# Optimization experiments

Hardware: AMD Instinct MI355X
Metric: run time of the kernel (lower is better)

Reference implementation:

```python
import jax, jax.numpy as jnp
import numpy as np

B, S, D = 4, 2048, 1024
H, DK, DV, DFF = 16, 64, 64, 4096
EPS = 1e-5


def layer_norm(x, g, b):
    mu = jnp.mean(x, axis=-1, keepdims=True)
    var = jnp.mean((x - mu) ** 2, axis=-1, keepdims=True)
    return (x - mu) * jax.lax.rsqrt(var + EPS) * g + b


def setup_inputs() -> dict:
    key = jax.random.key(0)
    ks = jax.random.split(key, 12)
    s = lambda fan_in: 1.0 / np.sqrt(fan_in)
    return {
        "x": jax.random.normal(ks[0], (B, S, D), dtype=jnp.float32),
        # per-head projections stacked: [H, D, DK/DV] (x @ W layout)
        "Wq": jax.random.normal(ks[1], (H, D, DK), dtype=jnp.float32) * s(D),
        "Wk": jax.random.normal(ks[2], (H, D, DK), dtype=jnp.float32) * s(D),
        "Wv": jax.random.normal(ks[3], (H, D, DV), dtype=jnp.float32) * s(D),
        "Wo": jax.random.normal(ks[4], (H * DV, D), dtype=jnp.float32) * s(H * DV),
        "ln1_g": jnp.ones((D,), dtype=jnp.float32),
        "ln1_b": jnp.zeros((D,), dtype=jnp.float32),
        "W1": jax.random.normal(ks[5], (D, DFF), dtype=jnp.float32) * s(D),
        "b1": jnp.zeros((DFF,), dtype=jnp.float32),
        "W2": jax.random.normal(ks[6], (DFF, D), dtype=jnp.float32) * s(DFF),
        "b2": jnp.zeros((D,), dtype=jnp.float32),
        "ln2_g": jnp.ones((D,), dtype=jnp.float32),
        "ln2_b": jnp.zeros((D,), dtype=jnp.float32),
    }


def reference(x, Wq, Wk, Wv, Wo, ln1_g, ln1_b, W1, b1, W2, b2, ln2_g, ln2_b):
    # --- multi-head causal self-attention (all heads vectorized) ---
    q = jnp.einsum("bsd,hdk->bhsk", x, Wq)
    k = jnp.einsum("bsd,hdk->bhsk", x, Wk)
    v = jnp.einsum("bsd,hdv->bhsv", x, Wv)
    # NOTE: original scales by 1/sqrt(x.shape[-1]) == 1/sqrt(d_model)
    scale = 1.0 / np.sqrt(D).astype(np.float32)
    scores = jnp.einsum("bhsk,bhtk->bhst", q, k) * scale  # [B,H,S,S]
    causal = jnp.tril(jnp.ones((S, S), dtype=bool))
    scores = jnp.where(causal, scores, -jnp.inf)
    attn = jax.nn.softmax(scores, axis=-1)
    ctx = jnp.einsum("bhst,bhtv->bhsv", attn, v)  # [B,H,S,DV]
    # concat heads (head-major last dim, matches torch.cat order)
    ctx = ctx.transpose(0, 2, 1, 3).reshape(B, S, H * DV)
    attn_out = ctx @ Wo  # [B,S,D]
    # Sublayer 1 (dropout is identity in eval)
    h1 = layer_norm(x + attn_out, ln1_g, ln1_b)
    # --- FFN ---
    ff = jax.nn.relu(h1 @ W1 + b1) @ W2 + b2
    # Sublayer 2
    return layer_norm(h1 + ff, ln2_g, ln2_b)
```

## Files before the change

### kernel.cpp

```cpp
#include <hip/hip_runtime.h>

#define DEV __device__ __forceinline__

using f16x8 = _Float16 __attribute__((ext_vector_type(8)));
using f16x4 = _Float16 __attribute__((ext_vector_type(4)));
using f32x4 = float __attribute__((ext_vector_type(4)));

DEV f32x4 mfma16(f16x8 a, f16x8 b, f32x4 c) {
    return __builtin_amdgcn_mfma_f32_16x16x32_f16(a, b, c, 0, 0, 0);
}

DEV void gload16(const void* g, void* l) {
    __builtin_amdgcn_global_load_lds(
        (const __attribute__((address_space(1))) void*)g,
        (__attribute__((address_space(3))) void*)l, 16, 0, 0);
}

template <int MODE>
__global__ __launch_bounds__(256, 2) void gemm_bt(
    const _Float16* __restrict__ A, const _Float16* __restrict__ Bt,
    int M, int N, int K,
    const float* __restrict__ ep0, const float* __restrict__ ep1,
    void* __restrict__ o0, void* __restrict__ o1, void* __restrict__ o2)
{
    __shared__ __align__(16) _Float16 As[128 * 64];
    __shared__ __align__(16) _Float16 Bs[128 * 64];
    const int tid  = threadIdx.x;
    const int wave = tid >> 6, lane = tid & 63;
    const int l16  = lane & 15, g = lane >> 4;
    const int m0 = blockIdx.x * 128, n0 = blockIdx.y * 128;
    const int wm = (wave >> 1) * 64, wn = (wave & 1) * 64;

    f32x4 acc[4][4] = {};

    for (int kt = 0; kt < K; kt += 64) {
#pragma unroll
        for (int it = 0; it < 4; ++it) {
            const int off  = it * 4096 + tid * 16;
            const int row  = off >> 7;
            const int colb = (off & 127) ^ ((row & 7) << 4);
            gload16(A + (size_t)(m0 + row) * K + kt + (colb >> 1), (char*)As + off);
        }
#pragma unroll
        for (int it = 0; it < 4; ++it) {
            const int off  = it * 4096 + tid * 16;
            const int row  = off >> 7;
            const int colb = (off & 127) ^ ((row & 7) << 4);
            gload16(Bt + (size_t)(n0 + row) * K + kt + (colb >> 1), (char*)Bs + off);
        }
        __syncthreads();
#pragma unroll
        for (int kk = 0; kk < 2; ++kk) {
            f16x8 af[4], bfv[4];
#pragma unroll
            for (int i = 0; i < 4; ++i) {
                const int ar = wm + i * 16 + l16;
                const int cb = ((kk * 32 + g * 8) << 1) ^ ((ar & 7) << 4);
                af[i] = *(const f16x8*)((const char*)As + (ar << 7) + cb);
            }
#pragma unroll
            for (int j = 0; j < 4; ++j) {
                const int br = wn + j * 16 + l16;
                const int cb = ((kk * 32 + g * 8) << 1) ^ ((br & 7) << 4);
                bfv[j] = *(const f16x8*)((const char*)Bs + (br << 7) + cb);
            }
#pragma unroll
            for (int i = 0; i < 4; ++i)
#pragma unroll
                for (int j = 0; j < 4; ++j)
                    acc[i][j] = mfma16(af[i], bfv[j], acc[i][j]);
        }
        __syncthreads();
    }

#pragma unroll
    for (int i = 0; i < 4; ++i) {
#pragma unroll
        for (int j = 0; j < 4; ++j) {
#pragma unroll
            for (int r = 0; r < 4; ++r) {
                const int m = m0 + wm + i * 16 + g * 4 + r;
                const int n = n0 + wn + j * 16 + l16;
                const float val = acc[i][j][r];
                if constexpr (MODE == 0) {
                    const int b = m >> 11, s = m & 2047;
                    const int which = n >> 10, hh = (n >> 6) & 15, dd = n & 63;
                    const size_t bh = (size_t)(b * 16 + hh);
                    if (which == 0) {
                        ((_Float16*)o0)[(bh * 2048 + s) * 64 + dd] =
                            (_Float16)(val * 0.04508422f);
                    } else if (which == 1) {
                        ((_Float16*)o1)[(bh * 2048 + s) * 64 + dd] = (_Float16)val;
                    } else {
                        ((_Float16*)o2)[(bh * 64 + dd) * 2048 + s] = (_Float16)val;
                    }
                } else if constexpr (MODE == 1) {
                    const size_t idx = (size_t)m * N + n;
                    ((float*)o0)[idx] = val + ep0[idx];
                } else if constexpr (MODE == 2) {
                    float v = val + ep0[n];
                    ((_Float16*)o0)[(size_t)m * N + n] = (_Float16)(v > 0.f ? v : 0.f);
                } else {
                    const size_t idx = (size_t)m * N + n;
                    ((float*)o0)[idx] = val + ep0[n] + ep1[idx];
                }
            }
        }
    }
}

DEV void stage_kv(const _Float16* __restrict__ Kh, const _Float16* __restrict__ Vh,
                  int kb0, char* ksb, char* vsb, int tid)
{
#pragma unroll
    for (int it = 0; it < 2; ++it) {
        const int off  = it * 4096 + tid * 16;
        const int row  = off >> 7;
        const int colb = (off & 127) ^ ((row & 7) << 4);
        gload16(Kh + (size_t)(kb0 + row) * 64 + (colb >> 1), ksb + off);
    }
#pragma unroll
    for (int it = 0; it < 2; ++it) {
        const int off  = it * 4096 + tid * 16;
        const int row  = off >> 7;
        const int colb = (off & 127) ^ ((row & 7) << 4);
        gload16(Vh + (size_t)row * 2048 + kb0 + (colb >> 1), vsb + off);
    }
}

__global__ __launch_bounds__(256, 4) void attn_kernel(
    const _Float16* __restrict__ Q, const _Float16* __restrict__ Kb,
    const _Float16* __restrict__ Vt, _Float16* __restrict__ ctx)
{
    __shared__ __align__(16) char smem[40960];
    const int tid = threadIdx.x;
    const int w = tid >> 6, lane = tid & 63;
    const int l16 = lane & 15, g = lane >> 4;
    const int bh = blockIdx.y;
    const int b = bh >> 4, h = bh & 15;
    const int tA = blockIdx.x;

    const _Float16* Kh = Kb + (size_t)bh * 2048 * 64;
    const _Float16* Vh = Vt + (size_t)bh * 64 * 2048;
    const int swl = (l16 & 7) << 4;
    char* prow = smem + 32768 + w * 2048 + l16 * 128;

    for (int half = 0; half < 2; ++half) {
        const int T = half ? (31 - tA) : tA;
        const int qbase = T * 64 + w * 16;
        const int qg = qbase + l16;
        const int nt = T + 1;

        const _Float16* qrow = Q + ((size_t)bh * 2048 + qg) * 64;
        const f16x8 qf0 = *(const f16x8*)(qrow + g * 8);
        const f16x8 qf1 = *(const f16x8*)(qrow + 32 + g * 8);

        f32x4 cacc[4] = {};
        float m_run = -INFINITY, l_run = 0.f;

        stage_kv(Kh, Vh, 0, smem, smem + 16384, tid);
        if (nt > 1) stage_kv(Kh, Vh, 64, smem + 8192, smem + 24576, tid);

        for (int kt = 0; kt < nt; ++kt) {
            const int bufo = (kt & 1) << 13;
            char* kbuf = smem + bufo;
            char* vbuf = smem + 16384 + bufo;

            if (kt + 1 < nt) asm volatile("s_waitcnt vmcnt(4)" ::: "memory");
            else             asm volatile("s_waitcnt vmcnt(0)" ::: "memory");
            __builtin_amdgcn_s_barrier();
            __builtin_amdgcn_sched_barrier(0);

            f32x4 st[4];
            __builtin_amdgcn_s_setprio(1);
#pragma unroll
            for (int s = 0; s < 4; ++s) {
                const char* kr = kbuf + (16 * s + l16) * 128;
                const f16x8 klo = *(const f16x8*)(kr + ((g * 16) ^ swl));
                const f16x8 khi = *(const f16x8*)(kr + ((64 + g * 16) ^ swl));
                f32x4 a0 = {0.f, 0.f, 0.f, 0.f};
                a0 = mfma16(klo, qf0, a0);
                st[s] = mfma16(khi, qf1, a0);
            }
            __builtin_amdgcn_s_setprio(0);

            if (kt == nt - 1) {
#pragma unroll
                for (int s = 0; s < 4; ++s)
#pragma unroll
                    for (int r = 0; r < 4; ++r) {
                        const int kg = kt * 64 + s * 16 + g * 4 + r;
                        if (kg > qg) st[s][r] = -INFINITY;
                    }
            }

            float tmax = st[0][0];
#pragma unroll
            for (int s = 0; s < 4; ++s)
#pragma unroll
                for (int r = 0; r < 4; ++r) tmax = fmaxf(tmax, st[s][r]);
            tmax = fmaxf(tmax, __shfl_xor(tmax, 16));
            tmax = fmaxf(tmax, __shfl_xor(tmax, 32));

            if (__any(tmax > m_run)) {
                const float m_new = fmaxf(m_run, tmax);
                const float alpha = exp2f(m_run - m_new);
                m_run = m_new;
                l_run *= alpha;
                f32x4 al;
#pragma unroll
                for (int r = 0; r < 4; ++r) al[r] = __shfl(alpha, g * 4 + r);
#pragma unroll
                for (int jt = 0; jt < 4; ++jt)
#pragma unroll
                    for (int r = 0; r < 4; ++r) cacc[jt][r] *= al[r];
            }

            float tsum = 0.f;
#pragma unroll
            for (int s = 0; s < 4; ++s) {
                f16x4 p;
#pragma unroll
                for (int r = 0; r < 4; ++r) {
                    const float e = exp2f(st[s][r] - m_run);
                    tsum += e;
                    p[r] = (_Float16)e;
                }
                *(f16x4*)(prow + ((s * 32 + g * 8) ^ swl)) = p;
            }
            tsum += __shfl_xor(tsum, 16);
            tsum += __shfl_xor(tsum, 32);
            l_run += tsum;

            const f16x8 pf0 = *(const f16x8*)(prow + ((g * 16) ^ swl));
            const f16x8 pf1 = *(const f16x8*)(prow + ((64 + g * 16) ^ swl));
            __builtin_amdgcn_s_setprio(1);
#pragma unroll
            for (int jt = 0; jt < 4; ++jt) {
                const char* vr = vbuf + (jt * 16 + l16) * 128;
                const f16x8 vlo = *(const f16x8*)(vr + ((g * 16) ^ swl));
                const f16x8 vhi = *(const f16x8*)(vr + ((64 + g * 16) ^ swl));
                cacc[jt] = mfma16(pf0, vlo, cacc[jt]);
                cacc[jt] = mfma16(pf1, vhi, cacc[jt]);
            }
            __builtin_amdgcn_s_setprio(0);

            __builtin_amdgcn_sched_barrier(0);
            __builtin_amdgcn_s_barrier();
            if (kt + 2 < nt)
                stage_kv(Kh, Vh, (kt + 2) * 64, kbuf, vbuf, tid);
        }

        __builtin_amdgcn_s_barrier();

        const float inv = 1.f / l_run;
        f32x4 il;
#pragma unroll
        for (int r = 0; r < 4; ++r) il[r] = __shfl(inv, g * 4 + r);
#pragma unroll
        for (int jt = 0; jt < 4; ++jt)
#pragma unroll
            for (int r = 0; r < 4; ++r)
                ctx[((size_t)b * 2048 + qbase + g * 4 + r) * 1024 + h * 64 + jt * 16 + l16]
                    = (_Float16)(cacc[jt][r] * il[r]);
    }
}

__global__ __launch_bounds__(256) void ln_kernel(
    const float* __restrict__ in, const float* __restrict__ gam, const float* __restrict__ bet,
    float* __restrict__ out32, _Float16* __restrict__ out16)
{
    const int row = blockIdx.x, tid = threadIdx.x;
    const float4 x = ((const float4*)(in + (size_t)row * 1024))[tid];
    float s  = x.x + x.y + x.z + x.w;
    float s2 = x.x * x.x + x.y * x.y + x.z * x.z + x.w * x.w;
#pragma unroll
    for (int o = 32; o > 0; o >>= 1) {
        s  += __shfl_xor(s, o);
        s2 += __shfl_xor(s2, o);
    }
    __shared__ float red[8];
    if ((tid & 63) == 0) { red[tid >> 6] = s; red[4 + (tid >> 6)] = s2; }
    __syncthreads();
    const float S  = red[0] + red[1] + red[2] + red[3];
    const float S2 = red[4] + red[5] + red[6] + red[7];
    const float mu = S * (1.f / 1024.f);
    const float ir = rsqrtf(S2 * (1.f / 1024.f) - mu * mu + 1e-5f);
    const float4 gv = ((const float4*)gam)[tid];
    const float4 bv = ((const float4*)bet)[tid];
    float4 o;
    o.x = (x.x - mu) * ir * gv.x + bv.x;
    o.y = (x.y - mu) * ir * gv.y + bv.y;
    o.z = (x.z - mu) * ir * gv.z + bv.z;
    o.w = (x.w - mu) * ir * gv.w + bv.w;
    if (out32) ((float4*)(out32 + (size_t)row * 1024))[tid] = o;
    if (out16) {
        f16x4 h;
        h[0] = (_Float16)o.x; h[1] = (_Float16)o.y; h[2] = (_Float16)o.z; h[3] = (_Float16)o.w;
        *(f16x4*)(out16 + (size_t)row * 1024 + tid * 4) = h;
    }
}

__global__ __launch_bounds__(256) void cast_f16(const float* __restrict__ in,
                                                _Float16* __restrict__ out, int n4)
{
    const int i = blockIdx.x * 256 + threadIdx.x;
    if (i < n4) {
        const float4 v = ((const float4*)in)[i];
        f16x4 h;
        h[0] = (_Float16)v.x; h[1] = (_Float16)v.y; h[2] = (_Float16)v.z; h[3] = (_Float16)v.w;
        ((f16x4*)out)[i] = h;
    }
}

__global__ __launch_bounds__(256) void transpose_cast(const float* __restrict__ src,
                                                      _Float16* __restrict__ dst, int K, int N)
{
    __shared__ float tile[64][65];
    const int n0 = blockIdx.x * 64, k0 = blockIdx.y * 64;
    const int tid = threadIdx.x;
#pragma unroll
    for (int it = 0; it < 16; ++it) {
        const int idx = it * 256 + tid;
        const int r = idx >> 6, c = idx & 63;
        tile[r][c] = src[(size_t)(k0 + r) * N + n0 + c];
    }
    __syncthreads();
#pragma unroll
    for (int it = 0; it < 16; ++it) {
        const int idx = it * 256 + tid;
        const int r = idx >> 6, c = idx & 63;
        dst[(size_t)(n0 + r) * K + k0 + c] = (_Float16)tile[c][r];
    }
}

__global__ __launch_bounds__(256) void pack_qkv_w(const float* __restrict__ Wq,
                                                  const float* __restrict__ Wk,
                                                  const float* __restrict__ Wv,
                                                  _Float16* __restrict__ dst)
{
    __shared__ float tile[64][65];
    const int n0 = blockIdx.x * 64, d0 = blockIdx.y * 64;
    const int which = n0 >> 10, hh = (n0 >> 6) & 15;
    const float* W = which == 0 ? Wq : (which == 1 ? Wk : Wv);
    const int tid = threadIdx.x;
#pragma unroll
    for (int it = 0; it < 16; ++it) {
        const int idx = it * 256 + tid;
        const int r = idx >> 6, c = idx & 63;
        tile[r][c] = W[((size_t)hh * 1024 + d0 + r) * 64 + c];
    }
    __syncthreads();
#pragma unroll
    for (int it = 0; it < 16; ++it) {
        const int idx = it * 256 + tid;
        const int r = idx >> 6, c = idx & 63;
        dst[(size_t)(n0 + r) * 1024 + d0 + c] = (_Float16)tile[c][r];
    }
}

extern "C" void kernel_launch(void* const* d_in, const int* in_sizes, int n_in,
                              void* d_out, int out_size, void* d_ws, size_t ws_size,
                              hipStream_t stream)
{
    const float* x    = (const float*)d_in[0];
    const float* Wq   = (const float*)d_in[1];
    const float* Wk   = (const float*)d_in[2];
    const float* Wv   = (const float*)d_in[3];
    const float* Wo   = (const float*)d_in[4];
    const float* ln1g = (const float*)d_in[5];
    const float* ln1b = (const float*)d_in[6];
    const float* W1   = (const float*)d_in[7];
    const float* b1   = (const float*)d_in[8];
    const float* W2   = (const float*)d_in[9];
    const float* b2   = (const float*)d_in[10];
    const float* ln2g = (const float*)d_in[11];
    const float* ln2b = (const float*)d_in[12];
    float* out = (float*)d_out;

    char* ws = (char*)d_ws;
    size_t off = 0;
    auto alloc = [&](size_t bytes) {
        void* p = ws + off;
        off += (bytes + 255) & ~(size_t)255;
        return p;
    };
    _Float16* x_h   = (_Float16*)alloc(8192ULL * 1024 * 2);
    _Float16* wqkv  = (_Float16*)alloc(3072ULL * 1024 * 2);
    _Float16* wo_t  = (_Float16*)alloc(1024ULL * 1024 * 2);
    _Float16* w1_t  = (_Float16*)alloc(4096ULL * 1024 * 2);
    _Float16* w2_t  = (_Float16*)alloc(1024ULL * 4096 * 2);
    _Float16* qbuf  = (_Float16*)alloc(8192ULL * 1024 * 2);
    _Float16* kbuf  = (_Float16*)alloc(8192ULL * 1024 * 2);
    _Float16* vt    = (_Float16*)alloc(8192ULL * 1024 * 2);
    _Float16* ctx   = (_Float16*)alloc(8192ULL * 1024 * 2);
    _Float16* ff1   = qbuf;
    float*    resid = (float*)alloc(8192ULL * 1024 * 4);
    float*    h1f   = (float*)alloc(8192ULL * 1024 * 4);
    _Float16* h1h   = (_Float16*)alloc(8192ULL * 1024 * 2);
    if (off > ws_size) return;

    cast_f16<<<8192, 256, 0, stream>>>(x, x_h, 2097152);
    pack_qkv_w<<<dim3(48, 16), 256, 0, stream>>>(Wq, Wk, Wv, wqkv);
    transpose_cast<<<dim3(16, 16), 256, 0, stream>>>(Wo, wo_t, 1024, 1024);
    transpose_cast<<<dim3(64, 16), 256, 0, stream>>>(W1, w1_t, 1024, 4096);
    transpose_cast<<<dim3(16, 64), 256, 0, stream>>>(W2, w2_t, 4096, 1024);

    gemm_bt<0><<<dim3(64, 24), 256, 0, stream>>>(x_h, wqkv, 8192, 3072, 1024,
                                                 nullptr, nullptr, qbuf, kbuf, vt);
    attn_kernel<<<dim3(16, 64), 256, 0, stream>>>(qbuf, kbuf, vt, ctx);
    gemm_bt<1><<<dim3(64, 8), 256, 0, stream>>>(ctx, wo_t, 8192, 1024, 1024,
                                                x, nullptr, resid, nullptr, nullptr);
    ln_kernel<<<8192, 256, 0, stream>>>(resid, ln1g, ln1b, h1f, h1h);
    gemm_bt<2><<<dim3(64, 32), 256, 0, stream>>>(h1h, w1_t, 8192, 4096, 1024,
                                                 b1, nullptr, ff1, nullptr, nullptr);
    gemm_bt<3><<<dim3(64, 8), 256, 0, stream>>>(ff1, w2_t, 8192, 1024, 4096,
                                                b2, h1f, resid, nullptr, nullptr);
    ln_kernel<<<8192, 256, 0, stream>>>(resid, ln2g, ln2b, out, nullptr);
}
```

Baseline: 395.1 us.

## Add 256x256-tile 4-stage pipelined GEMM for QKV and FFN1 projections

```diff
diff --git a/kernel.cpp b/kernel.cpp
--- a/kernel.cpp
+++ b/kernel.cpp
@@ -14,6 +14,111 @@
     __builtin_amdgcn_global_load_lds(
         (const __attribute__((address_space(1))) void*)g,
         (__attribute__((address_space(3))) void*)l, 16, 0, 0);
+}
+
+DEV void stage_sub(const _Float16* __restrict__ A, const _Float16* __restrict__ Bt,
+                   int K, int m0, int n0, int s, char* slot, int tid)
+{
+#pragma unroll
+    for (int p = 0; p < 2; ++p) {
+        const int off  = p * 8192 + tid * 16;
+        const int row  = off >> 6;
+        const int colb = (off & 63) ^ (((row >> 1) & 3) << 4);
+        gload16(A + (size_t)(m0 + row) * K + s * 32 + (colb >> 1), slot + off);
+    }
+#pragma unroll
+    for (int p = 0; p < 2; ++p) {
+        const int off  = p * 8192 + tid * 16;
+        const int row  = off >> 6;
+        const int colb = (off & 63) ^ (((row >> 1) & 3) << 4);
+        gload16(Bt + (size_t)(n0 + row) * K + s * 32 + (colb >> 1), slot + 16384 + off);
+    }
+}
+
+template <int MODE>
+__global__ __launch_bounds__(512, 2) void gemm256(
+    const _Float16* __restrict__ A, const _Float16* __restrict__ Bt,
+    int M, int N, int K,
+    const float* __restrict__ ep0,
+    void* __restrict__ o0, void* __restrict__ o1, void* __restrict__ o2)
+{
+    __shared__ __align__(16) char smem[131072];
+    const int tid = threadIdx.x;
+    const int wid = tid >> 6, lane = tid & 63;
+    const int l16 = lane & 15, g = lane >> 4;
+    const int wr = wid >> 2, wc = wid & 3;
+    const int m0 = blockIdx.x * 256, n0 = blockIdx.y * 256;
+    const int S = K >> 5;
+
+    f32x4 acc[8][4] = {};
+
+    const int swz   = ((l16 >> 1) & 3) << 4;
+    const int aoffb = (wr * 128 + l16) * 64 + ((g * 16) ^ swz);
+    const int boffb = 16384 + (wc * 64 + l16) * 64 + ((g * 16) ^ swz);
+
+    stage_sub(A, Bt, K, m0, n0, 0, smem, tid);
+    if (S > 1) stage_sub(A, Bt, K, m0, n0, 1, smem + 32768, tid);
+    if (S > 2) stage_sub(A, Bt, K, m0, n0, 2, smem + 65536, tid);
+
+    for (int s = 0; s < S; ++s) {
+        if (s + 3 <= S)      asm volatile("s_waitcnt vmcnt(8)" ::: "memory");
+        else if (s + 2 == S) asm volatile("s_waitcnt vmcnt(4)" ::: "memory");
+        else                 asm volatile("s_waitcnt vmcnt(0)" ::: "memory");
+        __builtin_amdgcn_s_barrier();
+        __builtin_amdgcn_sched_barrier(0);
+
+        char* slot = smem + ((s & 3) << 15);
+        if (s + 3 < S)
+            stage_sub(A, Bt, K, m0, n0, s + 3, smem + (((s + 3) & 3) << 15), tid);
+
+        f16x8 af[8], bf[4];
+#pragma unroll
+        for (int mi = 0; mi < 8; ++mi)
+            af[mi] = *(const f16x8*)(slot + aoffb + mi * 1024);
+#pragma unroll
+        for (int nj = 0; nj < 4; ++nj)
+            bf[nj] = *(const f16x8*)(slot + boffb + nj * 1024);
+        asm volatile("s_waitcnt lgkmcnt(0)" ::: "memory");
+        __builtin_amdgcn_sched_barrier(0);
+
+        __builtin_amdgcn_s_setprio(1);
+#pragma unroll
+        for (int mi = 0; mi < 8; ++mi)
+#pragma unroll
+            for (int nj = 0; nj < 4; ++nj)
+                acc[mi][nj] = mfma16(af[mi], bf[nj], acc[mi][nj]);
+        __builtin_amdgcn_s_setprio(0);
+        __builtin_amdgcn_sched_barrier(0);
+    }
+
+#pragma unroll
+    for (int mi = 0; mi < 8; ++mi) {
+#pragma unroll
+        for (int nj = 0; nj < 4; ++nj) {
+#pragma unroll
+            for (int r = 0; r < 4; ++r) {
+                const int m = m0 + wr * 128 + mi * 16 + g * 4 + r;
+                const int n = n0 + wc * 64 + nj * 16 + l16;
+                const float val = acc[mi][nj][r];
+                if constexpr (MODE == 0) {
+                    const int b = m >> 11, ss = m & 2047;
+                    const int which = n >> 10, hh = (n >> 6) & 15, dd = n & 63;
+                    const size_t bh = (size_t)(b * 16 + hh);
+                    if (which == 0) {
+                        ((_Float16*)o0)[(bh * 2048 + ss) * 64 + dd] =
+                            (_Float16)(val * 0.04508422f);
+                    } else if (which == 1) {
+                        ((_Float16*)o1)[(bh * 2048 + ss) * 64 + dd] = (_Float16)val;
+                    } else {
+                        ((_Float16*)o2)[(bh * 64 + dd) * 2048 + ss] = (_Float16)val;
+                    }
+                } else {
+                    float v = val + ep0[n];
+                    ((_Float16*)o0)[(size_t)m * N + n] = (_Float16)(v > 0.f ? v : 0.f);
+                }
+            }
+        }
+    }
 }
 
 template <int MODE>
@@ -21,7 +126,7 @@
     const _Float16* __restrict__ A, const _Float16* __restrict__ Bt,
     int M, int N, int K,
     const float* __restrict__ ep0, const float* __restrict__ ep1,
-    void* __restrict__ o0, void* __restrict__ o1, void* __restrict__ o2)
+    void* __restrict__ o0)
 {
     __shared__ __align__(16) _Float16 As[128 * 64];
     __shared__ __align__(16) _Float16 Bs[128 * 64];
@@ -82,24 +187,9 @@
                 const int m = m0 + wm + i * 16 + g * 4 + r;
                 const int n = n0 + wn + j * 16 + l16;
                 const float val = acc[i][j][r];
-                if constexpr (MODE == 0) {
-                    const int b = m >> 11, s = m & 2047;
-                    const int which = n >> 10, hh = (n >> 6) & 15, dd = n & 63;
-                    const size_t bh = (size_t)(b * 16 + hh);
-                    if (which == 0) {
-                        ((_Float16*)o0)[(bh * 2048 + s) * 64 + dd] =
-                            (_Float16)(val * 0.04508422f);
-                    } else if (which == 1) {
-                        ((_Float16*)o1)[(bh * 2048 + s) * 64 + dd] = (_Float16)val;
-                    } else {
-                        ((_Float16*)o2)[(bh * 64 + dd) * 2048 + s] = (_Float16)val;
-                    }
-                } else if constexpr (MODE == 1) {
+                if constexpr (MODE == 1) {
                     const size_t idx = (size_t)m * N + n;
                     ((float*)o0)[idx] = val + ep0[idx];
-                } else if constexpr (MODE == 2) {
-                    float v = val + ep0[n];
-                    ((_Float16*)o0)[(size_t)m * N + n] = (_Float16)(v > 0.f ? v : 0.f);
                 } else {
                     const size_t idx = (size_t)m * N + n;
                     ((float*)o0)[idx] = val + ep0[n] + ep1[idx];
@@ -204,7 +294,7 @@
 
             if (__any(tmax > m_run)) {
                 const float m_new = fmaxf(m_run, tmax);
-                const float alpha = exp2f(m_run - m_new);
+                const float alpha = __builtin_amdgcn_exp2f(m_run - m_new);
                 m_run = m_new;
                 l_run *= alpha;
                 f32x4 al;
@@ -222,7 +312,7 @@
                 f16x4 p;
 #pragma unroll
                 for (int r = 0; r < 4; ++r) {
-                    const float e = exp2f(st[s][r] - m_run);
+                    const float e = __builtin_amdgcn_exp2f(st[s][r] - m_run);
                     tsum += e;
                     p[r] = (_Float16)e;
                 }
@@ -406,15 +496,15 @@
     transpose_cast<<<dim3(64, 16), 256, 0, stream>>>(W1, w1_t, 1024, 4096);
     transpose_cast<<<dim3(16, 64), 256, 0, stream>>>(W2, w2_t, 4096, 1024);
 
-    gemm_bt<0><<<dim3(64, 24), 256, 0, stream>>>(x_h, wqkv, 8192, 3072, 1024,
-                                                 nullptr, nullptr, qbuf, kbuf, vt);
+    gemm256<0><<<dim3(32, 12), 512, 0, stream>>>(x_h, wqkv, 8192, 3072, 1024,
+                                                 nullptr, qbuf, kbuf, vt);
     attn_kernel<<<dim3(16, 64), 256, 0, stream>>>(qbuf, kbuf, vt, ctx);
     gemm_bt<1><<<dim3(64, 8), 256, 0, stream>>>(ctx, wo_t, 8192, 1024, 1024,
-                                                x, nullptr, resid, nullptr, nullptr);
+                                                x, nullptr, resid);
     ln_kernel<<<8192, 256, 0, stream>>>(resid, ln1g, ln1b, h1f, h1h);
-    gemm_bt<2><<<dim3(64, 32), 256, 0, stream>>>(h1h, w1_t, 8192, 4096, 1024,
-                                                 b1, nullptr, ff1, nullptr, nullptr);
+    gemm256<2><<<dim3(32, 16), 512, 0, stream>>>(h1h, w1_t, 8192, 4096, 1024,
+                                                 b1, ff1, nullptr, nullptr);
     gemm_bt<3><<<dim3(64, 8), 256, 0, stream>>>(ff1, w2_t, 8192, 1024, 4096,
-                                                b2, h1f, resid, nullptr, nullptr);
+                                                b2, h1f, resid);
     ln_kernel<<<8192, 256, 0, stream>>>(resid, ln2g, ln2b, out, nullptr);
 }
```

Result: slower. 415.9 us (+5.3%).
